# Kernel optimization log

Measured on AMD Instinct MI355X. Metric: run time of the kernel, lower is better.

Reference implementation:

```python
import jax, jax.numpy as jnp
import numpy as np

N_GROUPS = 4


def setup_inputs() -> dict:
    key = jax.random.key(0)
    ks = jax.random.split(key, 6)
    I, J, B = 512, 512, 4  # query tokens, key tokens, grid batch (B = 1 * n_groups)
    n_dim, out_per_group = 128, 4  # n_heads // n_groups = 16 // 4
    grid_q = jax.random.normal(ks[0], (I, 3), dtype=jnp.float32)
    grid_kv = jax.random.normal(ks[1], (B, J, 3), dtype=jnp.float32)
    W1 = jax.random.normal(ks[2], (3, n_dim), dtype=jnp.float32) * (1.0 / np.sqrt(3))
    b1 = jnp.zeros((n_dim,), dtype=jnp.float32)
    W2 = jax.random.normal(ks[3], (n_dim, n_dim), dtype=jnp.float32) * (1.0 / np.sqrt(n_dim))
    b2 = jnp.zeros((n_dim,), dtype=jnp.float32)
    W3 = jax.random.normal(ks[4], (n_dim, out_per_group), dtype=jnp.float32) * (1.0 / np.sqrt(n_dim))
    b3 = jnp.zeros((out_per_group,), dtype=jnp.float32)
    return {"grid_q": grid_q, "grid_kv": grid_kv, "W1": W1, "b1": b1,
            "W2": W2, "b2": b2, "W3": W3, "b3": b3}


def reference(grid_q, grid_kv, W1, b1, W2, b2, W3, b3):
    # grid_q: [I, 3] -> [1, I, 3]; grid_kv: [B, J, 3]
    gq = grid_q[None, :, :]
    # pairwise position difference: [B, I, J, 3]
    pos = gq[:, :, None, :] - grid_kv[:, None, :, :]
    # sign-log transform
    bias = jnp.sign(pos) * jnp.log1p(jnp.abs(pos))
    # tiny MLP: 3 -> n_dim -> n_dim -> heads//groups, pointwise over (B, I, J)
    h = jax.nn.relu(jnp.einsum('bijc,cd->bijd', bias, W1) + b1)
    h = jax.nn.relu(jnp.einsum('bijd,de->bije', h, W2) + b2)
    out = jnp.einsum('bije,eo->bijo', h, W3) + b3  # [B, I, J, O]
    # rearrange '(b g) i j o -> b (g o) i j' with g = N_GROUPS
    B, I, J, O = out.shape
    out = out.reshape(B // N_GROUPS, N_GROUPS, I, J, O)
    out = jnp.transpose(out, (0, 1, 4, 2, 3)).reshape(B // N_GROUPS, N_GROUPS * O, I, J)
    return out
```

## Files before the change

kernel.cpp:

```cpp
#include <hip/hip_runtime.h>
#include <math.h>

#define NBLOCKS 4096
#define THREADS 256
#define TILE 32
#define POS_PER_BLOCK 256
#define ITERS 8
#define CH 256

typedef __attribute__((ext_vector_type(8)))  short  short8;
typedef __attribute__((ext_vector_type(4)))  float  float4v;
typedef __attribute__((ext_vector_type(4)))  unsigned uint4v;
typedef __attribute__((ext_vector_type(16))) float  float16;

__device__ __forceinline__ unsigned cvt_pk(float lo, float hi) {
    unsigned r;
    asm("v_cvt_pk_bf16_f32 %0, %1, %2" : "=v"(r) : "v"(lo), "v"(hi));
    return r;
}

__device__ __forceinline__ int kmap(int c, int jj) {
    return 32 * (c >> 2) + 16 * ((c >> 1) & 1) + 4 * (c & 1) + ((jj >> 2) << 3) + (jj & 3);
}

__global__ __launch_bounds__(256, 4)
void crpb_mfma8(const float* __restrict__ gq,
                const float* __restrict__ gkv,
                const float* __restrict__ W1,
                const float* __restrict__ b1,
                const float* __restrict__ W2,
                const float* __restrict__ b2,
                const float* __restrict__ W3,
                const float* __restrict__ b3,
                float* __restrict__ out)
{
    __shared__ __align__(16) unsigned short ash[2][16 * CH];
    __shared__ __align__(16) float red[2][4 * 4 * 32];
    __shared__ __align__(16) float b2s[128];
    __shared__ __align__(16) unsigned fA[256][4];
    __shared__ __align__(16) unsigned fB[256];

    const int tid  = threadIdx.x;
    const int lane = tid & 63;
    const int w    = __builtin_amdgcn_readfirstlane(tid >> 6);
    const int l31  = lane & 31;
    const int lh   = lane >> 5;

    if (tid < 128) b2s[tid] = b2[tid];

    const int ct = w;

    float16 z16;
    #pragma unroll
    for (int r = 0; r < 16; ++r) z16[r] = 0.0f;

    short8 w1f;
    {
        const int ch = ct * 32 + l31;
        const float w0 = W1[ch], w1v = W1[128 + ch], w2v = W1[256 + ch], b1v = b1[ch];
        const float w0h = __uint_as_float(cvt_pk(w0, w0) << 16);
        const float w1h = __uint_as_float(cvt_pk(w1v, w1v) << 16);
        const float w2h = __uint_as_float(cvt_pk(w2v, w2v) << 16);
        const float b1h = __uint_as_float(cvt_pk(b1v, b1v) << 16);
        const float w0l = w0 - w0h, w1l = w1v - w1h, w2l = w2v - w2h, b1l = b1v - b1h;
        unsigned d[4];
        if (lh == 0) {
            d[0] = cvt_pk(w0h, w0l);
            d[1] = cvt_pk(w0h, w1h);
            d[2] = cvt_pk(w1l, w1h);
            d[3] = cvt_pk(w2h, w2l);
        } else {
            d[0] = cvt_pk(w2h, b1h);
            d[1] = cvt_pk(b1l, 0.0f);
            d[2] = 0; d[3] = 0;
        }
        __builtin_memcpy(&w1f, d, 16);
    }

    short8 a2f[8];
    {
        const int e = ct * 32 + l31;
        #pragma unroll
        for (int ks = 0; ks < 8; ++ks) {
            const int c = 2 * ks + lh;
            unsigned t0[4];
            #pragma unroll
            for (int t = 0; t < 4; ++t) {
                const int d0 = kmap(c, 2 * t), d1 = d0 + 1;
                t0[t] = cvt_pk(W2[d0 * 128 + e], W2[d1 * 128 + e]);
            }
            __builtin_memcpy(&a2f[ks], t0, 16);
        }
    }

    short8 w3a[2];
    #pragma unroll
    for (int m2 = 0; m2 < 2; ++m2) {
        unsigned tt[4];
        #pragma unroll
        for (int t = 0; t < 4; ++t) {
            const int chl = ((2 * t) & 3) + 8 * ((2 * t) >> 2) + 4 * lh + 16 * m2;
            const int ch0 = ct * 32 + chl, ch1 = ch0 + 1;
            const float lo = (l31 < 4) ? W3[ch0 * 4 + l31] : 0.0f;
            const float hi = (l31 < 4) ? W3[ch1 * 4 + l31] : 0.0f;
            tt[t] = cvt_pk(lo, hi);
        }
        __builtin_memcpy(&w3a[m2], tt, 16);
    }
    const float b3r = b3[w];

    const int posblock = blockIdx.x * POS_PER_BLOCK;
    const int bb    = posblock >> 18;
    const int i     = (posblock >> 9) & 511;
    const int jbase = posblock & 511;
    const float q0 = gq[i * 3 + 0], q1 = gq[i * 3 + 1], q2 = gq[i * 3 + 2];
    const float* kvrow = gkv + (size_t)((bb << 9) + jbase) * 3;

    {
        const int jj = tid;
        const float k0 = kvrow[jj * 3 + 0], k1 = kvrow[jj * 3 + 1], k2 = kvrow[jj * 3 + 2];
        const float c0 = q0 - k0, c1 = q1 - k1, c2 = q2 - k2;
        const float f0 = copysignf(__logf(1.0f + fabsf(c0)), c0);
        const float f1 = copysignf(__logf(1.0f + fabsf(c1)), c1);
        const float f2 = copysignf(__logf(1.0f + fabsf(c2)), c2);
        const unsigned u0 = cvt_pk(f0, f0), u2 = cvt_pk(f2, f2);
        const float f0h = __uint_as_float(u0 << 16);
        const float f1h = __uint_as_float(cvt_pk(f1, f1) << 16);
        const float f2h = __uint_as_float(u2 << 16);
        const float f0l = f0 - f0h, f1l = f1 - f1h, f2l = f2 - f2h;
        fA[jj][0] = u0;
        fA[jj][1] = cvt_pk(f0l, f1);
        fA[jj][2] = cvt_pk(f1, f1l);
        fA[jj][3] = u2;
        fB[jj]    = cvt_pk(f2l, 1.0f);
    }
    __syncthreads();

    auto phaseA = [&](int x, int buf) {
        const int jj = x * TILE + l31;
        unsigned d[4];
        if (lh == 0) {
            const uint4v t = *(const uint4v*)&fA[jj][0];
            d[0] = t[0]; d[1] = t[1]; d[2] = t[2]; d[3] = t[3];
        } else {
            d[0] = fB[jj];
            d[1] = 0x00003F80u;
            d[2] = 0; d[3] = 0;
        }
        short8 bf; __builtin_memcpy(&bf, d, 16);

        float16 c1r = __builtin_amdgcn_mfma_f32_32x32x16_bf16(w1f, bf, z16, 0, 0, 0);
        unsigned pk0[4], pk1[4];
        #pragma unroll
        for (int t = 0; t < 4; ++t) {
            pk0[t] = cvt_pk(fmaxf(c1r[2 * t], 0.f),     fmaxf(c1r[2 * t + 1], 0.f));
            pk1[t] = cvt_pk(fmaxf(c1r[8 + 2 * t], 0.f), fmaxf(c1r[8 + 2 * t + 1], 0.f));
        }
        short8 v0, v1;
        __builtin_memcpy(&v0, pk0, 16);
        __builtin_memcpy(&v1, pk1, 16);
        *(short8*)&ash[buf][(4 * ct + lh) * CH + l31 * 8]     = v0;
        *(short8*)&ash[buf][(4 * ct + 2 + lh) * CH + l31 * 8] = v1;
    };

    phaseA(0, 0);
    __syncthreads();

    for (int it = 0; it < ITERS; ++it) {
        const int buf = it & 1;
        const int jb = jbase + it * TILE;

        float16 acc;
        #pragma unroll
        for (int qr = 0; qr < 4; ++qr) {
            float4v i0 = *(const float4v*)&b2s[ct * 32 + 8 * qr + 4 * lh];
            #pragma unroll
            for (int t = 0; t < 4; ++t) acc[4 * qr + t] = i0[t];
        }
        const unsigned short* br = &ash[buf][lh * CH + l31 * 8];

        __builtin_amdgcn_s_setprio(1);
        #pragma unroll
        for (int ks = 0; ks < 8; ++ks) {
            short8 bfrag = *(const short8*)(br + ks * 2 * CH);
            acc = __builtin_amdgcn_mfma_f32_32x32x16_bf16(a2f[ks], bfrag, acc, 0, 0, 0);
        }

        {
            unsigned pa0[4], pa1[4];
            #pragma unroll
            for (int t = 0; t < 4; ++t) {
                pa0[t] = cvt_pk(fmaxf(acc[2 * t], 0.f),     fmaxf(acc[2 * t + 1], 0.f));
                pa1[t] = cvt_pk(fmaxf(acc[8 + 2 * t], 0.f), fmaxf(acc[8 + 2 * t + 1], 0.f));
            }
            short8 fa0, fa1;
            __builtin_memcpy(&fa0, pa0, 16); __builtin_memcpy(&fa1, pa1, 16);
            float16 p;
            p = __builtin_amdgcn_mfma_f32_32x32x16_bf16(w3a[0], fa0, z16, 0, 0, 0);
            p = __builtin_amdgcn_mfma_f32_32x32x16_bf16(w3a[1], fa1, p, 0, 0, 0);
            __builtin_amdgcn_s_setprio(0);
            if (lh == 0) {
                #pragma unroll
                for (int o = 0; o < 4; ++o)
                    red[buf][ct * 128 + o * 32 + l31] = p[o];
            }
        }

        if (it != ITERS - 1) phaseA(it + 1, 1 - buf);

        __syncthreads();

        if (lh == 0) {
            const int o = w, pos = l31;
            const float v = b3r
                          + red[buf][0 * 128 + o * 32 + pos]
                          + red[buf][1 * 128 + o * 32 + pos]
                          + red[buf][2 * 128 + o * 32 + pos]
                          + red[buf][3 * 128 + o * 32 + pos];
            out[((size_t)((bb << 2) + o) << 18) + ((size_t)i << 9) + jb + pos] = v;
        }
    }
}

extern "C" void kernel_launch(void* const* d_in, const int* in_sizes, int n_in,
                              void* d_out, int out_size, void* d_ws, size_t ws_size,
                              hipStream_t stream) {
    const float* gq  = (const float*)d_in[0];
    const float* gkv = (const float*)d_in[1];
    const float* W1  = (const float*)d_in[2];
    const float* b1  = (const float*)d_in[3];
    const float* W2  = (const float*)d_in[4];
    const float* b2  = (const float*)d_in[5];
    const float* W3  = (const float*)d_in[6];
    const float* b3  = (const float*)d_in[7];
    float* out = (float*)d_out;

    crpb_mfma8<<<NBLOCKS, THREADS, 0, stream>>>(gq, gkv, W1, b1, W2, b2, W3, b3, out);
}
```

Measured before the change: 121.8 us.

## Give each wave whole position tiles and stage W2/W3 fragments in LDS

Work is now split across waves by position tile rather than by output channel slice. Each wave handles two 32-position tiles end to end through all four channel slices, so the cross-wave LDS reduction and the per-iteration block barriers go away. The W2 and W3 MFMA fragments move from registers into shared memory, read once per MFMA, and launch bounds drop to 3 blocks per CU to leave room for the larger LDS footprint and registers. In exchange there are many more LDS reads per MFMA and lower occupancy.

```diff
diff --git a/kernel.cpp b/kernel.cpp
--- a/kernel.cpp
+++ b/kernel.cpp
@@ -3,10 +3,7 @@
 
 #define NBLOCKS 4096
 #define THREADS 256
-#define TILE 32
 #define POS_PER_BLOCK 256
-#define ITERS 8
-#define CH 256
 
 typedef __attribute__((ext_vector_type(8)))  short  short8;
 typedef __attribute__((ext_vector_type(4)))  float  float4v;
@@ -23,7 +20,7 @@
     return 32 * (c >> 2) + 16 * ((c >> 1) & 1) + 4 * (c & 1) + ((jj >> 2) << 3) + (jj & 3);
 }
 
-__global__ __launch_bounds__(256, 4)
+__global__ __launch_bounds__(256, 3)
 void crpb_mfma8(const float* __restrict__ gq,
                 const float* __restrict__ gkv,
                 const float* __restrict__ W1,
@@ -34,11 +31,11 @@
                 const float* __restrict__ b3,
                 float* __restrict__ out)
 {
-    __shared__ __align__(16) unsigned short ash[2][16 * CH];
-    __shared__ __align__(16) float red[2][4 * 4 * 32];
-    __shared__ __align__(16) float b2s[128];
+    __shared__ __align__(16) unsigned w2l[2048][4];
+    __shared__ __align__(16) unsigned w3l[512][4];
     __shared__ __align__(16) unsigned fA[256][4];
     __shared__ __align__(16) unsigned fB[256];
+    __shared__ __align__(16) float b2s[128];
 
     const int tid  = threadIdx.x;
     const int lane = tid & 63;
@@ -48,66 +45,65 @@
 
     if (tid < 128) b2s[tid] = b2[tid];
 
-    const int ct = w;
-
     float16 z16;
     #pragma unroll
     for (int r = 0; r < 16; ++r) z16[r] = 0.0f;
 
-    short8 w1f;
-    {
-        const int ch = ct * 32 + l31;
+    short8 w1f[4];
+    #pragma unroll
+    for (int et = 0; et < 4; ++et) {
+        const int ch = et * 32 + l31;
         const float w0 = W1[ch], w1v = W1[128 + ch], w2v = W1[256 + ch], b1v = b1[ch];
         const float w0h = __uint_as_float(cvt_pk(w0, w0) << 16);
         const float w1h = __uint_as_float(cvt_pk(w1v, w1v) << 16);
         const float w2h = __uint_as_float(cvt_pk(w2v, w2v) << 16);
         const float b1h = __uint_as_float(cvt_pk(b1v, b1v) << 16);
-        const float w0l = w0 - w0h, w1l = w1v - w1h, w2l = w2v - w2h, b1l = b1v - b1h;
+        const float w0l = w0 - w0h, w1l = w1v - w1h, w2l_ = w2v - w2h, b1l = b1v - b1h;
         unsigned d[4];
         if (lh == 0) {
             d[0] = cvt_pk(w0h, w0l);
             d[1] = cvt_pk(w0h, w1h);
             d[2] = cvt_pk(w1l, w1h);
-            d[3] = cvt_pk(w2h, w2l);
+            d[3] = cvt_pk(w2h, w2l_);
         } else {
             d[0] = cvt_pk(w2h, b1h);
             d[1] = cvt_pk(b1l, 0.0f);
             d[2] = 0; d[3] = 0;
         }
-        __builtin_memcpy(&w1f, d, 16);
-    }
-
-    short8 a2f[8];
-    {
-        const int e = ct * 32 + l31;
-        #pragma unroll
-        for (int ks = 0; ks < 8; ++ks) {
-            const int c = 2 * ks + lh;
-            unsigned t0[4];
-            #pragma unroll
-            for (int t = 0; t < 4; ++t) {
-                const int d0 = kmap(c, 2 * t), d1 = d0 + 1;
-                t0[t] = cvt_pk(W2[d0 * 128 + e], W2[d1 * 128 + e]);
-            }
-            __builtin_memcpy(&a2f[ks], t0, 16);
-        }
-    }
-
-    short8 w3a[2];
-    #pragma unroll
-    for (int m2 = 0; m2 < 2; ++m2) {
-        unsigned tt[4];
+        __builtin_memcpy(&w1f[et], d, 16);
+    }
+
+    for (int s = tid; s < 2048; s += THREADS) {
+        const int ln   = s & 63;
+        const int ks   = (s >> 6) & 7;
+        const int et   = s >> 9;
+        const int lh_t = ln >> 5;
+        const int e    = et * 32 + (ln & 31);
+        const int c    = 2 * ks + lh_t;
         #pragma unroll
         for (int t = 0; t < 4; ++t) {
-            const int chl = ((2 * t) & 3) + 8 * ((2 * t) >> 2) + 4 * lh + 16 * m2;
-            const int ch0 = ct * 32 + chl, ch1 = ch0 + 1;
-            const float lo = (l31 < 4) ? W3[ch0 * 4 + l31] : 0.0f;
-            const float hi = (l31 < 4) ? W3[ch1 * 4 + l31] : 0.0f;
-            tt[t] = cvt_pk(lo, hi);
-        }
-        __builtin_memcpy(&w3a[m2], tt, 16);
-    }
-    const float b3r = b3[w];
+            const int d0 = kmap(c, 2 * t);
+            w2l[s][t] = cvt_pk(W2[d0 * 128 + e], W2[(d0 + 1) * 128 + e]);
+        }
+    }
+
+    for (int s = tid; s < 512; s += THREADS) {
+        const int ln   = s & 63;
+        const int m2   = (s >> 6) & 1;
+        const int et   = s >> 7;
+        const int lh_t = ln >> 5;
+        const int l31t = ln & 31;
+        #pragma unroll
+        for (int t = 0; t < 4; ++t) {
+            const int chl = ((2 * t) & 3) + 8 * ((2 * t) >> 2) + 4 * lh_t + 16 * m2;
+            const int ch0 = et * 32 + chl;
+            const float lo = (l31t < 4) ? W3[ch0 * 4 + l31t] : 0.0f;
+            const float hi = (l31t < 4) ? W3[(ch0 + 1) * 4 + l31t] : 0.0f;
+            w3l[s][t] = cvt_pk(lo, hi);
+        }
+    }
+
+    const float b3v0 = b3[0], b3v1 = b3[1], b3v2 = b3[2], b3v3 = b3[3];
 
     const int posblock = blockIdx.x * POS_PER_BLOCK;
     const int bb    = posblock >> 18;
@@ -134,10 +130,14 @@
         fA[jj][3] = u2;
         fB[jj]    = cvt_pk(f2l, 1.0f);
     }
+
     __syncthreads();
 
-    auto phaseA = [&](int x, int buf) {
-        const int jj = x * TILE + l31;
+    #pragma unroll
+    for (int t8 = 0; t8 < 2; ++t8) {
+        const int tile = w * 2 + t8;
+        const int jj   = tile * 32 + l31;
+
         unsigned d[4];
         if (lh == 0) {
             const uint4v t = *(const uint4v*)&fA[jj][0];
@@ -149,44 +149,37 @@
         }
         short8 bf; __builtin_memcpy(&bf, d, 16);
 
-        float16 c1r = __builtin_amdgcn_mfma_f32_32x32x16_bf16(w1f, bf, z16, 0, 0, 0);
-        unsigned pk0[4], pk1[4];
-        #pragma unroll
-        for (int t = 0; t < 4; ++t) {
-            pk0[t] = cvt_pk(fmaxf(c1r[2 * t], 0.f),     fmaxf(c1r[2 * t + 1], 0.f));
-            pk1[t] = cvt_pk(fmaxf(c1r[8 + 2 * t], 0.f), fmaxf(c1r[8 + 2 * t + 1], 0.f));
-        }
-        short8 v0, v1;
-        __builtin_memcpy(&v0, pk0, 16);
-        __builtin_memcpy(&v1, pk1, 16);
-        *(short8*)&ash[buf][(4 * ct + lh) * CH + l31 * 8]     = v0;
-        *(short8*)&ash[buf][(4 * ct + 2 + lh) * CH + l31 * 8] = v1;
-    };
-
-    phaseA(0, 0);
-    __syncthreads();
-
-    for (int it = 0; it < ITERS; ++it) {
-        const int buf = it & 1;
-        const int jb = jbase + it * TILE;
-
-        float16 acc;
-        #pragma unroll
-        for (int qr = 0; qr < 4; ++qr) {
-            float4v i0 = *(const float4v*)&b2s[ct * 32 + 8 * qr + 4 * lh];
-            #pragma unroll
-            for (int t = 0; t < 4; ++t) acc[4 * qr + t] = i0[t];
-        }
-        const unsigned short* br = &ash[buf][lh * CH + l31 * 8];
-
+        short8 h1f[4][2];
         __builtin_amdgcn_s_setprio(1);
         #pragma unroll
-        for (int ks = 0; ks < 8; ++ks) {
-            short8 bfrag = *(const short8*)(br + ks * 2 * CH);
-            acc = __builtin_amdgcn_mfma_f32_32x32x16_bf16(a2f[ks], bfrag, acc, 0, 0, 0);
-        }
-
-        {
+        for (int et = 0; et < 4; ++et) {
+            float16 c1r = __builtin_amdgcn_mfma_f32_32x32x16_bf16(w1f[et], bf, z16, 0, 0, 0);
+            unsigned pk0[4], pk1[4];
+            #pragma unroll
+            for (int t = 0; t < 4; ++t) {
+                pk0[t] = cvt_pk(fmaxf(c1r[2 * t], 0.f),     fmaxf(c1r[2 * t + 1], 0.f));
+                pk1[t] = cvt_pk(fmaxf(c1r[8 + 2 * t], 0.f), fmaxf(c1r[8 + 2 * t + 1], 0.f));
+            }
+            __builtin_memcpy(&h1f[et][0], pk0, 16);
+            __builtin_memcpy(&h1f[et][1], pk1, 16);
+        }
+
+        float16 p;
+        #pragma unroll
+        for (int et = 0; et < 4; ++et) {
+            float16 acc;
+            #pragma unroll
+            for (int qr = 0; qr < 4; ++qr) {
+                const float4v bv = *(const float4v*)&b2s[et * 32 + 8 * qr + 4 * lh];
+                #pragma unroll
+                for (int t = 0; t < 4; ++t) acc[4 * qr + t] = bv[t];
+            }
+            #pragma unroll
+            for (int ks = 0; ks < 8; ++ks) {
+                const uint4v wv = *(const uint4v*)&w2l[(et * 8 + ks) * 64 + lane][0];
+                short8 af; __builtin_memcpy(&af, &wv, 16);
+                acc = __builtin_amdgcn_mfma_f32_32x32x16_bf16(af, h1f[ks >> 1][ks & 1], acc, 0, 0, 0);
+            }
             unsigned pa0[4], pa1[4];
             #pragma unroll
             for (int t = 0; t < 4; ++t) {
@@ -195,29 +188,22 @@
             }
             short8 fa0, fa1;
             __builtin_memcpy(&fa0, pa0, 16); __builtin_memcpy(&fa1, pa1, 16);
-            float16 p;
-            p = __builtin_amdgcn_mfma_f32_32x32x16_bf16(w3a[0], fa0, z16, 0, 0, 0);
-            p = __builtin_amdgcn_mfma_f32_32x32x16_bf16(w3a[1], fa1, p, 0, 0, 0);
-            __builtin_amdgcn_s_setprio(0);
-            if (lh == 0) {
-                #pragma unroll
-                for (int o = 0; o < 4; ++o)
-                    red[buf][ct * 128 + o * 32 + l31] = p[o];
-            }
-        }
-
-        if (it != ITERS - 1) phaseA(it + 1, 1 - buf);
-
-        __syncthreads();
+            const uint4v w30 = *(const uint4v*)&w3l[(et * 2 + 0) * 64 + lane][0];
+            const uint4v w31 = *(const uint4v*)&w3l[(et * 2 + 1) * 64 + lane][0];
+            short8 a30, a31;
+            __builtin_memcpy(&a30, &w30, 16); __builtin_memcpy(&a31, &w31, 16);
+            if (et == 0) p = __builtin_amdgcn_mfma_f32_32x32x16_bf16(a30, fa0, z16, 0, 0, 0);
+            else         p = __builtin_amdgcn_mfma_f32_32x32x16_bf16(a30, fa0, p,   0, 0, 0);
+            p = __builtin_amdgcn_mfma_f32_32x32x16_bf16(a31, fa1, p, 0, 0, 0);
+        }
+        __builtin_amdgcn_s_setprio(0);
 
         if (lh == 0) {
-            const int o = w, pos = l31;
-            const float v = b3r
-                          + red[buf][0 * 128 + o * 32 + pos]
-                          + red[buf][1 * 128 + o * 32 + pos]
-                          + red[buf][2 * 128 + o * 32 + pos]
-                          + red[buf][3 * 128 + o * 32 + pos];
-            out[((size_t)((bb << 2) + o) << 18) + ((size_t)i << 9) + jb + pos] = v;
+            const size_t base = ((size_t)(bb << 2) << 18) + ((size_t)i << 9) + jbase + tile * 32 + l31;
+            out[base + ((size_t)0 << 18)] = p[0] + b3v0;
+            out[base + ((size_t)1 << 18)] = p[1] + b3v1;
+            out[base + ((size_t)2 << 18)] = p[2] + b3v2;
+            out[base + ((size_t)3 << 18)] = p[3] + b3v3;
         }
     }
 }
```

Result: slower. 125.9 us (+3.3%).
